# Optimization experiments

Hardware: AMD Instinct MI355X
Metric: run time of the kernel (lower is better)

Reference implementation:

```python
import jax, jax.numpy as jnp
import numpy as np

EMBED_DIM = 1024
NUM_HEADS = 16
HEAD_DIM = EMBED_DIM // NUM_HEADS


def setup_inputs() -> dict:
    key = jax.random.key(0)
    ks = jax.random.split(key, 9)
    s = 1.0 / np.sqrt(EMBED_DIM)
    inp = {"x": jax.random.normal(ks[0], (2, 2048, EMBED_DIM), dtype=jnp.float32)}
    for i, name in enumerate(["q", "k", "v", "out"]):
        inp[f"W_{name}"] = jax.random.uniform(ks[1 + 2 * i], (EMBED_DIM, EMBED_DIM), jnp.float32, -s, s)
        inp[f"b_{name}"] = jax.random.uniform(ks[2 + 2 * i], (EMBED_DIM,), jnp.float32, -s, s)
    return inp


def _heads(x):
    # [B, S, D] -> [B, H, S, Dh]
    b, s, _ = x.shape
    return x.reshape(b, s, NUM_HEADS, HEAD_DIM).transpose(0, 2, 1, 3)


def reference(x, W_q, b_q, W_k, b_k, W_v, b_v, W_out, b_out):
    q = _heads(x @ W_q.T + b_q)
    k = _heads(x @ W_k.T + b_k)
    v = _heads(x @ W_v.T + b_v)
    scale = HEAD_DIM ** 0.5
    logits = jnp.einsum("bhqd,bhkd->bhqk", q, k) / scale  # [B,H,S,S]
    s = x.shape[1]
    causal = jnp.tril(jnp.ones((s, s), dtype=bool))
    logits = jnp.where(causal, logits, -jnp.inf)
    a = jax.nn.softmax(logits, axis=-1)
    o = jnp.einsum("bhqk,bhkd->bhqd", a, v)
    o = o.transpose(0, 2, 1, 3).reshape(x.shape[0], s, EMBED_DIM)
    return o @ W_out.T + b_out
```

## Files before the change

### kernel.cpp

```cpp
#include <hip/hip_runtime.h>
#include <hip/hip_bf16.h>

typedef __bf16 bf16_t;
typedef __bf16 bf16x8 __attribute__((ext_vector_type(8)));
typedef __bf16 bf16x4 __attribute__((ext_vector_type(4)));
typedef float  f32x4  __attribute__((ext_vector_type(4)));

#define MFMA16(a, b, c) __builtin_amdgcn_mfma_f32_16x16x32_bf16((a), (b), (c), 0, 0, 0)

constexpr int E  = 1024;
constexpr int S  = 2048;
constexpr int H  = 16;
constexpr int M  = 4096;

__device__ __forceinline__ void glds16(const bf16_t* src, bf16_t* dst) {
  __builtin_amdgcn_global_load_lds(
      (const __attribute__((address_space(1))) void*)src,
      (__attribute__((address_space(3))) void*)dst, 16, 0, 0);
}

template <int ROWS, int NT>
__device__ __forceinline__ void stage_tile(const bf16_t* g, int gld,
                                           bf16_t* lds, int tid) {
  const int w = tid >> 6, l = tid & 63;
#pragma unroll
  for (int i = 0; i < ROWS * 8 / NT; ++i) {
    const int c = i * NT + w * 64 + l;
    const int row = c >> 3;
    const int gch = (c & 7) ^ (row & 7);
    glds16(g + (size_t)row * gld + gch * 8, lds + (size_t)(i * NT + w * 64) * 8);
  }
}

__device__ __forceinline__ void stage_v128(const bf16_t* g, int gld,
                                           bf16_t* lds, int tid) {
#pragma unroll
  for (int i = 0; i < 4; ++i) {
    const int c = i * 256 + tid;
    const int row = c >> 4, col16 = c & 15;
    const int gch = col16 ^ (row & 7);
    glds16(g + (size_t)row * gld + gch * 8, lds + (size_t)c * 8);
  }
}

__device__ __forceinline__ void stage_A_chunk(const bf16_t* g, int c,
                                              bf16_t* lds, int tid) {
  const int w = tid >> 6, l = tid & 63;
#pragma unroll
  for (int i = 0; i < 2; ++i) {
    const int gc = i * 512 + w * 64 + l;
    const int row_l = gc >> 3;
    const int col8 = gc & 7;
    const int h = row_l >> 6, rr = row_l & 63;
    const int row = h * 128 + c * 64 + rr;
    const int gch = col8 ^ (row & 7);
    glds16(g + (size_t)row * E + gch * 8, lds + ((size_t)row * 8 + col8) * 8);
  }
}

__device__ __forceinline__ bf16x8 read_frag(const bf16_t* lds, int row, int kc) {
  return *(const bf16x8*)(lds + (size_t)((row << 3) + (kc ^ (row & 7))) * 8);
}

__device__ __forceinline__ bf16x8 read_v128(const bf16_t* lds, int row, int kc) {
  return *(const bf16x8*)(lds + (size_t)((row << 4) + (kc ^ (row & 7))) * 8);
}

__global__ void cvt_all_kernel(const float* __restrict__ x,
                               const float* __restrict__ w0, const float* __restrict__ w1,
                               const float* __restrict__ w2, const float* __restrict__ w3,
                               bf16_t* __restrict__ xb,
                               bf16_t* __restrict__ o0, bf16_t* __restrict__ o1,
                               bf16_t* __restrict__ o2, bf16_t* __restrict__ o3) {
  const int bid = blockIdx.x;
  const float* s;
  bf16_t* d;
  int idx;
  if (bid < 4096) {
    s = x; d = xb; idx = bid * 256 + threadIdx.x;
  } else {
    const int seg = (bid - 4096) >> 10;
    s = seg == 0 ? w0 : seg == 1 ? w1 : seg == 2 ? w2 : w3;
    d = seg == 0 ? o0 : seg == 1 ? o1 : seg == 2 ? o2 : o3;
    idx = ((bid - 4096) & 1023) * 256 + threadIdx.x;
  }
  float4 v = ((const float4*)s)[idx];
  bf16x4 o;
  o[0] = (bf16_t)v.x; o[1] = (bf16_t)v.y; o[2] = (bf16_t)v.z; o[3] = (bf16_t)v.w;
  ((bf16x4*)d)[idx] = o;
}

__global__ __launch_bounds__(512, 1) void qkv8_kernel(
    const bf16_t* __restrict__ xb, const bf16_t* __restrict__ W3,
    const float* __restrict__ bq, const float* __restrict__ bk,
    const float* __restrict__ bv, bf16_t* __restrict__ QKb,
    bf16_t* __restrict__ VT) {
  __shared__ __align__(16) bf16_t As[2][256 * 64];
  __shared__ __align__(16) bf16_t Bs[2][256 * 64];
  const int tid = threadIdx.x;
  const int l = tid & 63, lq = l & 15, qd = l >> 4;
  const int w = tid >> 6, wm = w >> 2, wn = w & 3;

  const int swz = (blockIdx.x & 7) * 24 + (blockIdx.x >> 3);
  const int by = swz / 12, bx = swz % 12;
  const int m0 = by * 256, n0 = bx * 256;

  const bf16_t* Ag = xb + (size_t)m0 * E;
  const bf16_t* Bg = W3 + (size_t)n0 * E;

  f32x4 acc[8][4];
#pragma unroll
  for (int jj = 0; jj < 8; ++jj)
#pragma unroll
    for (int n = 0; n < 4; ++n) acc[jj][n] = (f32x4){0.f, 0.f, 0.f, 0.f};

  stage_tile<128, 512>(Bg, E, Bs[0], tid);
  stage_tile<128, 512>(Bg + (size_t)128 * E, E, Bs[0] + 128 * 64, tid);
  stage_A_chunk(Ag, 0, As[0], tid);
  stage_A_chunk(Ag, 1, As[0], tid);
  asm volatile("s_waitcnt vmcnt(2)" ::: "memory");
  __builtin_amdgcn_s_barrier();

#pragma unroll 1
  for (int g = 0; g < 16; ++g) {
    const int s = g & 1;
    const bf16_t* Al = As[s];
    const bf16_t* Bl = Bs[s];
    bf16_t* An = As[s ^ 1];
    bf16_t* Bn = Bs[s ^ 1];
    const bf16_t* Agn = Ag + (g + 1) * 64;
    const bf16_t* Bgn = Bg + (g + 1) * 64;
    const bool more = (g < 15);
    bf16x8 af[4], bfr[4];

#pragma unroll
    for (int jj = 0; jj < 4; ++jj)
      af[jj] = read_frag(Al, wm * 128 + jj * 16 + lq, qd);
#pragma unroll
    for (int n = 0; n < 4; ++n)
      bfr[n] = read_frag(Bl, wn * 64 + n * 16 + lq, qd);
    if (more) stage_tile<128, 512>(Bgn, E, Bn, tid);
    __builtin_amdgcn_s_barrier();
    asm volatile("s_waitcnt lgkmcnt(0)" ::: "memory");
    __builtin_amdgcn_sched_barrier(0);
    __builtin_amdgcn_s_setprio(1);
#pragma unroll
    for (int jj = 0; jj < 4; ++jj)
#pragma unroll
      for (int n = 0; n < 4; ++n)
        acc[jj][n] = MFMA16(af[jj], bfr[n], acc[jj][n]);
    __builtin_amdgcn_s_setprio(0);
    if (more) asm volatile("s_waitcnt vmcnt(2)" ::: "memory");
    else      asm volatile("s_waitcnt vmcnt(0)" ::: "memory");
    __builtin_amdgcn_s_barrier();

#pragma unroll
    for (int jj = 0; jj < 4; ++jj)
      af[jj] = read_frag(Al, wm * 128 + (4 + jj) * 16 + lq, qd);
    if (more) stage_tile<128, 512>(Bgn + (size_t)128 * E, E, Bn + 128 * 64, tid);
    __builtin_amdgcn_s_barrier();
    asm volatile("s_waitcnt lgkmcnt(0)" ::: "memory");
    __builtin_amdgcn_sched_barrier(0);
    __builtin_amdgcn_s_setprio(1);
#pragma unroll
    for (int jj = 0; jj < 4; ++jj)
#pragma unroll
      for (int n = 0; n < 4; ++n)
        acc[4 + jj][n] = MFMA16(af[jj], bfr[n], acc[4 + jj][n]);
    __builtin_amdgcn_s_setprio(0);
    __builtin_amdgcn_s_barrier();

#pragma unroll
    for (int jj = 0; jj < 4; ++jj)
      af[jj] = read_frag(Al, wm * 128 + jj * 16 + lq, 4 + qd);
#pragma unroll
    for (int n = 0; n < 4; ++n)
      bfr[n] = read_frag(Bl, wn * 64 + n * 16 + lq, 4 + qd);
    if (more) stage_A_chunk(Agn, 0, An, tid);
    __builtin_amdgcn_s_barrier();
    asm volatile("s_waitcnt lgkmcnt(0)" ::: "memory");
    __builtin_amdgcn_sched_barrier(0);
    __builtin_amdgcn_s_setprio(1);
#pragma unroll
    for (int jj = 0; jj < 4; ++jj)
#pragma unroll
      for (int n = 0; n < 4; ++n)
        acc[jj][n] = MFMA16(af[jj], bfr[n], acc[jj][n]);
    __builtin_amdgcn_s_setprio(0);
    __builtin_amdgcn_s_barrier();

#pragma unroll
    for (int jj = 0; jj < 4; ++jj)
      af[jj] = read_frag(Al, wm * 128 + (4 + jj) * 16 + lq, 4 + qd);
    if (more) stage_A_chunk(Agn, 1, An, tid);
    __builtin_amdgcn_s_barrier();
    asm volatile("s_waitcnt lgkmcnt(0)" ::: "memory");
    __builtin_amdgcn_sched_barrier(0);
    __builtin_amdgcn_s_setprio(1);
#pragma unroll
    for (int jj = 0; jj < 4; ++jj)
#pragma unroll
      for (int n = 0; n < 4; ++n)
        acc[4 + jj][n] = MFMA16(af[jj], bfr[n], acc[4 + jj][n]);
    __builtin_amdgcn_s_setprio(0);
    if (more) asm volatile("s_waitcnt vmcnt(2)" ::: "memory");
    __builtin_amdgcn_s_barrier();
  }

  const int mat = n0 >> 10;
  const int ccb = n0 & 1023;
  const float* bp = (mat == 0) ? bq : (mat == 1) ? bk : bv;
  if (mat < 2) {
    const float sc = (mat == 0) ? 0.18033688011112043f : 1.0f;
    bf16_t* Out = QKb + (size_t)mat * ((size_t)M * E);
#pragma unroll
    for (int n = 0; n < 4; ++n) {
      const int cc = ccb + wn * 64 + n * 16 + lq;
      const float bvv = bp[cc];
#pragma unroll
      for (int jj = 0; jj < 8; ++jj)
#pragma unroll
        for (int r = 0; r < 4; ++r) {
          const int row = m0 + wm * 128 + jj * 16 + qd * 4 + r;
          Out[(size_t)row * E + cc] = (bf16_t)((acc[jj][n][r] + bvv) * sc);
        }
    }
  } else {
#pragma unroll
    for (int n = 0; n < 4; ++n) {
      const int cc = ccb + wn * 64 + n * 16 + lq;
      const float bvv = bp[cc];
      const int d = cc & 63, hh = cc >> 6;
#pragma unroll
      for (int jj = 0; jj < 8; ++jj) {
        const int row = m0 + wm * 128 + jj * 16 + qd * 4;
        const int bb_ = row >> 11;
        const int s_loc = row & (S - 1);
        const int sl = s_loc & 63, s0 = s_loc & ~63;
        const int a = sl >> 4, b4 = (sl >> 2) & 3;
        const int pb = (a >> 1) * 32 + b4 * 8 + (a & 1) * 4;
        bf16x4 vv;
#pragma unroll
        for (int r = 0; r < 4; ++r) vv[r] = (bf16_t)(acc[jj][n][r] + bvv);
        *(bf16x4*)&VT[((size_t)((bb_ * 16 + hh) * 64 + d)) * S + s0 + pb] = vv;
      }
    }
  }
}

__global__ __launch_bounds__(256) void oproj_gemm_kernel(
    const bf16_t* __restrict__ Ob, const bf16_t* __restrict__ wo,
    const float* __restrict__ bo, float* __restrict__ out) {
  __shared__ __align__(16) bf16_t As[64 * 64];
  __shared__ __align__(16) bf16_t Bs[128 * 64];
  const int tid = threadIdx.x;
  const int n0 = blockIdx.x * 128;
  const int m0 = blockIdx.y * 64;
  const int w = tid >> 6, l = tid & 63, lq = l & 15, qd = l >> 4;
  const int wr = (w >> 1) * 32, wc = (w & 1) * 64;

  f32x4 acc[2][4];
#pragma unroll
  for (int i = 0; i < 2; ++i)
#pragma unroll
    for (int j = 0; j < 4; ++j) acc[i][j] = (f32x4){0.f, 0.f, 0.f, 0.f};

  for (int kt = 0; kt < 16; ++kt) {
    __syncthreads();
    stage_tile<64, 256>(Ob + (size_t)m0 * E + kt * 64, E, As, tid);
    stage_tile<128, 256>(wo + (size_t)n0 * E + kt * 64, E, Bs, tid);
    __syncthreads();
#pragma unroll
    for (int ks = 0; ks < 2; ++ks) {
      bf16x8 af[2], bw[4];
#pragma unroll
      for (int mi = 0; mi < 2; ++mi)
        af[mi] = read_frag(As, wr + mi * 16 + lq, ks * 4 + qd);
#pragma unroll
      for (int ni = 0; ni < 4; ++ni)
        bw[ni] = read_frag(Bs, wc + ni * 16 + lq, ks * 4 + qd);
#pragma unroll
      for (int mi = 0; mi < 2; ++mi)
#pragma unroll
        for (int ni = 0; ni < 4; ++ni)
          acc[mi][ni] = MFMA16(af[mi], bw[ni], acc[mi][ni]);
    }
  }
#pragma unroll
  for (int ni = 0; ni < 4; ++ni) {
    const int col = n0 + wc + ni * 16 + lq;
    const float bvv = bo[col];
#pragma unroll
    for (int mi = 0; mi < 2; ++mi)
#pragma unroll
      for (int r = 0; r < 4; ++r) {
        const int row = m0 + wr + mi * 16 + qd * 4 + r;
        out[(size_t)row * E + col] = acc[mi][ni][r] + bvv;
      }
  }
}

__global__ __launch_bounds__(256, 2) void attn_kernel(
    const bf16_t* __restrict__ Q, const bf16_t* __restrict__ K,
    const bf16_t* __restrict__ VT, bf16_t* __restrict__ O) {
  __shared__ __align__(16) bf16_t Ks[2][128 * 64];
  __shared__ __align__(16) bf16_t Vt[2][64 * 128];

  const int tid = threadIdx.x;
  const int w = tid >> 6, l = tid & 63;
  const int lq = l & 15, qd = l >> 4;
  const int bid = blockIdx.x;
  const int g = bid & 7, t = bid >> 3;
  const int bh = g * 4 + (t & 3);
  const int p = t >> 2;
  const int b = bh >> 4, h = bh & 15;
  const size_t rowbase = (size_t)b * S;
  const bf16_t* Kg = K + rowbase * E + h * 64;
  const bf16_t* Vg = VT + (size_t)bh * 64 * S;

  stage_tile<128, 256>(Kg, E, Ks[0], tid);
  stage_v128(Vg, S, Vt[0], tid);
  int cb = 0;

#pragma unroll 1
  for (int seg = 0; seg < 2; ++seg) {
    const int qt = seg ? p : 31 - p;
    const int T = (qt + 2) >> 1;
    const int qr = qt * 64 + w * 16;
    const int qg = qr + lq;

    bf16x8 aq[2];
#pragma unroll
    for (int ks = 0; ks < 2; ++ks)
      aq[ks] = *(const bf16x8*)(Q + (rowbase + qr + lq) * E + h * 64 +
                                ks * 32 + qd * 8);

    f32x4 oacc[4];
#pragma unroll
    for (int nt = 0; nt < 4; ++nt) oacc[nt] = (f32x4){0.f, 0.f, 0.f, 0.f};
    float rs4[4] = {0.f, 0.f, 0.f, 0.f};

    for (int kt = 0; kt < T; ++kt) {
      __syncthreads();
      if (kt < T - 1) {
        const int kn = (kt + 1) * 128;
        stage_tile<128, 256>(Kg + (size_t)kn * E, E, Ks[cb ^ 1], tid);
        stage_v128(Vg + kn, S, Vt[cb ^ 1], tid);
      } else if (seg == 0) {
        stage_tile<128, 256>(Kg, E, Ks[cb ^ 1], tid);
        stage_v128(Vg, S, Vt[cb ^ 1], tid);
      }
      const bf16_t* Kc = Ks[cb];
      const bf16_t* Vc = Vt[cb];
      const int k0 = kt * 128;
      const bool needmask = (kt == T - 1);

      f32x4 sacc[8];
#pragma unroll
      for (int nt = 0; nt < 8; ++nt) sacc[nt] = (f32x4){0.f, 0.f, 0.f, 0.f};
      __builtin_amdgcn_s_setprio(1);
#pragma unroll
      for (int ks = 0; ks < 2; ++ks) {
        bf16x8 bk[8];
#pragma unroll
        for (int nt = 0; nt < 8; ++nt)
          bk[nt] = read_frag(Kc, nt * 16 + lq, ks * 4 + qd);
#pragma unroll
        for (int nt = 0; nt < 8; ++nt)
          sacc[nt] = MFMA16(bk[nt], aq[ks], sacc[nt]);
      }
      __builtin_amdgcn_s_setprio(0);

      bf16x8 ap[4];
      if (needmask) {
#pragma unroll
        for (int nt = 0; nt < 8; ++nt)
#pragma unroll
          for (int r = 0; r < 4; ++r) {
            float pv = __builtin_amdgcn_exp2f(sacc[nt][r]);
            const int kg = k0 + nt * 16 + qd * 4 + r;
            pv = (kg > qg) ? 0.f : pv;
            rs4[nt & 3] += pv;
            ap[nt >> 1][((nt & 1) << 2) | r] = (bf16_t)pv;
          }
      } else {
#pragma unroll
        for (int nt = 0; nt < 8; ++nt)
#pragma unroll
          for (int r = 0; r < 4; ++r) {
            float pv = __builtin_amdgcn_exp2f(sacc[nt][r]);
            rs4[nt & 3] += pv;
            ap[nt >> 1][((nt & 1) << 2) | r] = (bf16_t)pv;
          }
      }

      __builtin_amdgcn_s_setprio(1);
#pragma unroll
      for (int c = 0; c < 4; ++c) {
        bf16x8 bv[4];
#pragma unroll
        for (int nt = 0; nt < 4; ++nt)
          bv[nt] = read_v128(Vc, nt * 16 + lq, c * 4 + qd);
#pragma unroll
        for (int nt = 0; nt < 4; ++nt)
          oacc[nt] = MFMA16(ap[c], bv[nt], oacc[nt]);
      }
      __builtin_amdgcn_s_setprio(0);
      cb ^= 1;
    }

    float rs = (rs4[0] + rs4[1]) + (rs4[2] + rs4[3]);
    rs += __shfl_xor(rs, 16);
    rs += __shfl_xor(rs, 32);
    float rinv[4];
#pragma unroll
    for (int r = 0; r < 4; ++r) rinv[r] = 1.0f / __shfl(rs, qd * 4 + r);
#pragma unroll
    for (int nt = 0; nt < 4; ++nt)
#pragma unroll
      for (int r = 0; r < 4; ++r) {
        const int qgw = qr + qd * 4 + r;
        O[(rowbase + qgw) * E + h * 64 + nt * 16 + lq] =
            (bf16_t)(oacc[nt][r] * rinv[r]);
      }
  }
}

extern "C" void kernel_launch(void* const* d_in, const int* in_sizes, int n_in,
                              void* d_out, int out_size, void* d_ws, size_t ws_size,
                              hipStream_t stream) {
  const float* x  = (const float*)d_in[0];
  const float* Wq = (const float*)d_in[1];
  const float* bq = (const float*)d_in[2];
  const float* Wk = (const float*)d_in[3];
  const float* bk = (const float*)d_in[4];
  const float* Wv = (const float*)d_in[5];
  const float* bv = (const float*)d_in[6];
  const float* Wo = (const float*)d_in[7];
  const float* bo = (const float*)d_in[8];
  float* out = (float*)d_out;

  unsigned char* ws = (unsigned char*)d_ws;
  constexpr size_t MB = 1ull << 20;
  bf16_t* xb  = (bf16_t*)(ws + 0 * MB);
  bf16_t* wqb = (bf16_t*)(ws + 8 * MB);
  bf16_t* wkb = (bf16_t*)(ws + 10 * MB);
  bf16_t* wvb = (bf16_t*)(ws + 12 * MB);
  bf16_t* wob = (bf16_t*)(ws + 14 * MB);
  bf16_t* Qb  = (bf16_t*)(ws + 16 * MB);
  bf16_t* VT  = (bf16_t*)(ws + 40 * MB);
  bf16_t* Ob  = xb;

  cvt_all_kernel<<<4096 + 4 * 1024, 256, 0, stream>>>(
      x, Wq, Wk, Wv, Wo, xb, wqb, wkb, wvb, wob);

  qkv8_kernel<<<192, 512, 0, stream>>>(xb, wqb, bq, bk, bv, Qb, VT);

  attn_kernel<<<512, 256, 0, stream>>>(Qb, Qb + (size_t)M * E, VT, Ob);

  oproj_gemm_kernel<<<dim3(8, 64), 256, 0, stream>>>(Ob, wob, bo, out);
}
```

Baseline: 173.8 us.

## Retile QKV GEMM to 256x192 over 256 blocks and software-pipeline attention PV

The QKV projection GEMM tile becomes 256x192, giving 256 workgroups instead of 192 to fill all CUs, with an XCD-aware region swizzle for L2 locality. The attention kernel now defers the P·V MFMAs by one iteration so they overlap with the next QK^T and exp work, using a triple-buffered V tile. It also computes the softmax row sums with an MFMA against a ones vector instead of VALU adds and cross-lane shuffles. The cost is more LDS for V, extra MFMA work for the row sums, and a more complex wait-count schedule.

```diff
diff --git a/kernel.cpp b/kernel.cpp
--- a/kernel.cpp
+++ b/kernel.cpp
@@ -96,26 +96,31 @@
     const float* __restrict__ bv, bf16_t* __restrict__ QKb,
     bf16_t* __restrict__ VT) {
   __shared__ __align__(16) bf16_t As[2][256 * 64];
-  __shared__ __align__(16) bf16_t Bs[2][256 * 64];
+  __shared__ __align__(16) bf16_t Bs[2][192 * 64];
   const int tid = threadIdx.x;
   const int l = tid & 63, lq = l & 15, qd = l >> 4;
   const int w = tid >> 6, wm = w >> 2, wn = w & 3;
 
-  const int swz = (blockIdx.x & 7) * 24 + (blockIdx.x >> 3);
-  const int by = swz / 12, bx = swz % 12;
-  const int m0 = by * 256, n0 = bx * 256;
+  const int wg = blockIdx.x;
+  const int xcd = wg & 7, i5 = wg >> 3;
+  const int region = xcd * 2 + (i5 >> 4);
+  const int j = i5 & 15;
+  const int bx = (region & 3) * 4 + (j & 3);
+  const int by = (region >> 2) * 4 + (j >> 2);
+  const int m0 = by * 256, n0 = bx * 192;
 
   const bf16_t* Ag = xb + (size_t)m0 * E;
   const bf16_t* Bg = W3 + (size_t)n0 * E;
 
-  f32x4 acc[8][4];
+  f32x4 acc[8][3];
 #pragma unroll
   for (int jj = 0; jj < 8; ++jj)
 #pragma unroll
-    for (int n = 0; n < 4; ++n) acc[jj][n] = (f32x4){0.f, 0.f, 0.f, 0.f};
-
-  stage_tile<128, 512>(Bg, E, Bs[0], tid);
-  stage_tile<128, 512>(Bg + (size_t)128 * E, E, Bs[0] + 128 * 64, tid);
+    for (int n = 0; n < 3; ++n) acc[jj][n] = (f32x4){0.f, 0.f, 0.f, 0.f};
+
+  stage_tile<64, 512>(Bg, E, Bs[0], tid);
+  stage_tile<64, 512>(Bg + (size_t)64 * E, E, Bs[0] + 64 * 64, tid);
+  stage_tile<64, 512>(Bg + (size_t)128 * E, E, Bs[0] + 128 * 64, tid);
   stage_A_chunk(Ag, 0, As[0], tid);
   stage_A_chunk(Ag, 1, As[0], tid);
   asm volatile("s_waitcnt vmcnt(2)" ::: "memory");
@@ -131,15 +136,15 @@
     const bf16_t* Agn = Ag + (g + 1) * 64;
     const bf16_t* Bgn = Bg + (g + 1) * 64;
     const bool more = (g < 15);
-    bf16x8 af[4], bfr[4];
+    bf16x8 af[4], bfr[3];
 
 #pragma unroll
     for (int jj = 0; jj < 4; ++jj)
       af[jj] = read_frag(Al, wm * 128 + jj * 16 + lq, qd);
 #pragma unroll
-    for (int n = 0; n < 4; ++n)
-      bfr[n] = read_frag(Bl, wn * 64 + n * 16 + lq, qd);
-    if (more) stage_tile<128, 512>(Bgn, E, Bn, tid);
+    for (int n = 0; n < 3; ++n)
+      bfr[n] = read_frag(Bl, wn * 48 + n * 16 + lq, qd);
+    if (more) stage_tile<64, 512>(Bgn, E, Bn, tid);
     __builtin_amdgcn_s_barrier();
     asm volatile("s_waitcnt lgkmcnt(0)" ::: "memory");
     __builtin_amdgcn_sched_barrier(0);
@@ -147,17 +152,17 @@
 #pragma unroll
     for (int jj = 0; jj < 4; ++jj)
 #pragma unroll
-      for (int n = 0; n < 4; ++n)
+      for (int n = 0; n < 3; ++n)
         acc[jj][n] = MFMA16(af[jj], bfr[n], acc[jj][n]);
     __builtin_amdgcn_s_setprio(0);
-    if (more) asm volatile("s_waitcnt vmcnt(2)" ::: "memory");
+    if (more) asm volatile("s_waitcnt vmcnt(1)" ::: "memory");
     else      asm volatile("s_waitcnt vmcnt(0)" ::: "memory");
     __builtin_amdgcn_s_barrier();
 
 #pragma unroll
     for (int jj = 0; jj < 4; ++jj)
       af[jj] = read_frag(Al, wm * 128 + (4 + jj) * 16 + lq, qd);
-    if (more) stage_tile<128, 512>(Bgn + (size_t)128 * E, E, Bn + 128 * 64, tid);
+    if (more) stage_tile<64, 512>(Bgn + (size_t)64 * E, E, Bn + 64 * 64, tid);
     __builtin_amdgcn_s_barrier();
     asm volatile("s_waitcnt lgkmcnt(0)" ::: "memory");
     __builtin_amdgcn_sched_barrier(0);
@@ -165,7 +170,7 @@
 #pragma unroll
     for (int jj = 0; jj < 4; ++jj)
 #pragma unroll
-      for (int n = 0; n < 4; ++n)
+      for (int n = 0; n < 3; ++n)
         acc[4 + jj][n] = MFMA16(af[jj], bfr[n], acc[4 + jj][n]);
     __builtin_amdgcn_s_setprio(0);
     __builtin_amdgcn_s_barrier();
@@ -174,9 +179,12 @@
     for (int jj = 0; jj < 4; ++jj)
       af[jj] = read_frag(Al, wm * 128 + jj * 16 + lq, 4 + qd);
 #pragma unroll
-    for (int n = 0; n < 4; ++n)
-      bfr[n] = read_frag(Bl, wn * 64 + n * 16 + lq, 4 + qd);
-    if (more) stage_A_chunk(Agn, 0, An, tid);
+    for (int n = 0; n < 3; ++n)
+      bfr[n] = read_frag(Bl, wn * 48 + n * 16 + lq, 4 + qd);
+    if (more) {
+      stage_tile<64, 512>(Bgn + (size_t)128 * E, E, Bn + 128 * 64, tid);
+      stage_A_chunk(Agn, 0, An, tid);
+    }
     __builtin_amdgcn_s_barrier();
     asm volatile("s_waitcnt lgkmcnt(0)" ::: "memory");
     __builtin_amdgcn_sched_barrier(0);
@@ -184,7 +192,7 @@
 #pragma unroll
     for (int jj = 0; jj < 4; ++jj)
 #pragma unroll
-      for (int n = 0; n < 4; ++n)
+      for (int n = 0; n < 3; ++n)
         acc[jj][n] = MFMA16(af[jj], bfr[n], acc[jj][n]);
     __builtin_amdgcn_s_setprio(0);
     __builtin_amdgcn_s_barrier();
@@ -200,23 +208,21 @@
 #pragma unroll
     for (int jj = 0; jj < 4; ++jj)
 #pragma unroll
-      for (int n = 0; n < 4; ++n)
+      for (int n = 0; n < 3; ++n)
         acc[4 + jj][n] = MFMA16(af[jj], bfr[n], acc[4 + jj][n]);
     __builtin_amdgcn_s_setprio(0);
     if (more) asm volatile("s_waitcnt vmcnt(2)" ::: "memory");
     __builtin_amdgcn_s_barrier();
   }
 
-  const int mat = n0 >> 10;
-  const int ccb = n0 & 1023;
-  const float* bp = (mat == 0) ? bq : (mat == 1) ? bk : bv;
-  if (mat < 2) {
-    const float sc = (mat == 0) ? 0.18033688011112043f : 1.0f;
-    bf16_t* Out = QKb + (size_t)mat * ((size_t)M * E);
-#pragma unroll
-    for (int n = 0; n < 4; ++n) {
-      const int cc = ccb + wn * 64 + n * 16 + lq;
-      const float bvv = bp[cc];
+#pragma unroll
+  for (int n = 0; n < 3; ++n) {
+    const int col = n0 + wn * 48 + n * 16 + lq;
+    const int mat = col >> 10, cc = col & 1023;
+    const float bvv = (mat == 0 ? bq : mat == 1 ? bk : bv)[cc];
+    if (mat < 2) {
+      const float sc = (mat == 0) ? 0.18033688011112043f : 1.0f;
+      bf16_t* Out = QKb + (size_t)mat * ((size_t)M * E);
 #pragma unroll
       for (int jj = 0; jj < 8; ++jj)
 #pragma unroll
@@ -224,12 +230,7 @@
           const int row = m0 + wm * 128 + jj * 16 + qd * 4 + r;
           Out[(size_t)row * E + cc] = (bf16_t)((acc[jj][n][r] + bvv) * sc);
         }
-    }
-  } else {
-#pragma unroll
-    for (int n = 0; n < 4; ++n) {
-      const int cc = ccb + wn * 64 + n * 16 + lq;
-      const float bvv = bp[cc];
+    } else {
       const int d = cc & 63, hh = cc >> 6;
 #pragma unroll
       for (int jj = 0; jj < 8; ++jj) {
@@ -304,7 +305,7 @@
     const bf16_t* __restrict__ Q, const bf16_t* __restrict__ K,
     const bf16_t* __restrict__ VT, bf16_t* __restrict__ O) {
   __shared__ __align__(16) bf16_t Ks[2][128 * 64];
-  __shared__ __align__(16) bf16_t Vt[2][64 * 128];
+  __shared__ __align__(16) bf16_t Vt[3][64 * 128];
 
   const int tid = threadIdx.x;
   const int w = tid >> 6, l = tid & 63;
@@ -318,9 +319,13 @@
   const bf16_t* Kg = K + rowbase * E + h * 64;
   const bf16_t* Vg = VT + (size_t)bh * 64 * S;
 
+  bf16x8 ones;
+#pragma unroll
+  for (int jj = 0; jj < 8; ++jj) ones[jj] = (bf16_t)1.0f;
+
   stage_tile<128, 256>(Kg, E, Ks[0], tid);
   stage_v128(Vg, S, Vt[0], tid);
-  int cb = 0;
+  int cb = 0, vcur = 0;
 
 #pragma unroll 1
   for (int seg = 0; seg < 2; ++seg) {
@@ -338,20 +343,36 @@
     f32x4 oacc[4];
 #pragma unroll
     for (int nt = 0; nt < 4; ++nt) oacc[nt] = (f32x4){0.f, 0.f, 0.f, 0.f};
-    float rs4[4] = {0.f, 0.f, 0.f, 0.f};
+    f32x4 osum = (f32x4){0.f, 0.f, 0.f, 0.f};
+    bf16x8 ap_prev[4];
+    int vprev = vcur;
+
+    auto do_pv = [&](const bf16_t* Vp) {
+#pragma unroll
+      for (int c = 0; c < 4; ++c) {
+        bf16x8 bv[4];
+#pragma unroll
+        for (int nt = 0; nt < 4; ++nt)
+          bv[nt] = read_v128(Vp, nt * 16 + lq, c * 4 + qd);
+#pragma unroll
+        for (int nt = 0; nt < 4; ++nt)
+          oacc[nt] = MFMA16(ap_prev[c], bv[nt], oacc[nt]);
+        osum = MFMA16(ap_prev[c], ones, osum);
+      }
+    };
 
     for (int kt = 0; kt < T; ++kt) {
       __syncthreads();
+      const int vnext = (vcur + 1 == 3) ? 0 : vcur + 1;
       if (kt < T - 1) {
         const int kn = (kt + 1) * 128;
         stage_tile<128, 256>(Kg + (size_t)kn * E, E, Ks[cb ^ 1], tid);
-        stage_v128(Vg + kn, S, Vt[cb ^ 1], tid);
+        stage_v128(Vg + kn, S, Vt[vnext], tid);
       } else if (seg == 0) {
         stage_tile<128, 256>(Kg, E, Ks[cb ^ 1], tid);
-        stage_v128(Vg, S, Vt[cb ^ 1], tid);
+        stage_v128(Vg, S, Vt[vnext], tid);
       }
       const bf16_t* Kc = Ks[cb];
-      const bf16_t* Vc = Vt[cb];
       const int k0 = kt * 128;
       const bool needmask = (kt == T - 1);
 
@@ -369,9 +390,9 @@
         for (int nt = 0; nt < 8; ++nt)
           sacc[nt] = MFMA16(bk[nt], aq[ks], sacc[nt]);
       }
+      if (kt > 0) do_pv(Vt[vprev]);
       __builtin_amdgcn_s_setprio(0);
 
-      bf16x8 ap[4];
       if (needmask) {
 #pragma unroll
         for (int nt = 0; nt < 8; ++nt)
@@ -380,8 +401,7 @@
             float pv = __builtin_amdgcn_exp2f(sacc[nt][r]);
             const int kg = k0 + nt * 16 + qd * 4 + r;
             pv = (kg > qg) ? 0.f : pv;
-            rs4[nt & 3] += pv;
-            ap[nt >> 1][((nt & 1) << 2) | r] = (bf16_t)pv;
+            ap_prev[nt >> 1][((nt & 1) << 2) | r] = (bf16_t)pv;
           }
       } else {
 #pragma unroll
@@ -389,32 +409,18 @@
 #pragma unroll
           for (int r = 0; r < 4; ++r) {
             float pv = __builtin_amdgcn_exp2f(sacc[nt][r]);
-            rs4[nt & 3] += pv;
-            ap[nt >> 1][((nt & 1) << 2) | r] = (bf16_t)pv;
+            ap_prev[nt >> 1][((nt & 1) << 2) | r] = (bf16_t)pv;
           }
       }
-
-      __builtin_amdgcn_s_setprio(1);
-#pragma unroll
-      for (int c = 0; c < 4; ++c) {
-        bf16x8 bv[4];
-#pragma unroll
-        for (int nt = 0; nt < 4; ++nt)
-          bv[nt] = read_v128(Vc, nt * 16 + lq, c * 4 + qd);
-#pragma unroll
-        for (int nt = 0; nt < 4; ++nt)
-          oacc[nt] = MFMA16(ap[c], bv[nt], oacc[nt]);
-      }
-      __builtin_amdgcn_s_setprio(0);
+      vprev = vcur;
+      vcur = vnext;
       cb ^= 1;
     }
-
-    float rs = (rs4[0] + rs4[1]) + (rs4[2] + rs4[3]);
-    rs += __shfl_xor(rs, 16);
-    rs += __shfl_xor(rs, 32);
+    do_pv(Vt[vprev]);
+
     float rinv[4];
 #pragma unroll
-    for (int r = 0; r < 4; ++r) rinv[r] = 1.0f / __shfl(rs, qd * 4 + r);
+    for (int r = 0; r < 4; ++r) rinv[r] = 1.0f / osum[r];
 #pragma unroll
     for (int nt = 0; nt < 4; ++nt)
 #pragma unroll
@@ -454,7 +460,7 @@
   cvt_all_kernel<<<4096 + 4 * 1024, 256, 0, stream>>>(
       x, Wq, Wk, Wv, Wo, xb, wqb, wkb, wvb, wob);
 
-  qkv8_kernel<<<192, 512, 0, stream>>>(xb, wqb, bq, bk, bv, Qb, VT);
+  qkv8_kernel<<<256, 512, 0, stream>>>(xb, wqb, bq, bk, bv, Qb, VT);
 
   attn_kernel<<<512, 256, 0, stream>>>(Qb, Qb + (size_t)M * E, VT, Ob);
 
```

Measured after the change: 171.8 us. Within noise of the previous version (-1.2%).
